# Performance work log

Hardware: AMD Instinct MI355X
Metric: run time of the kernel (lower is better)

The kernel has to match this reference:

```python
import jax, jax.numpy as jnp
import numpy as np

DIM = 768
HEADS = 12
HEAD_DIM = DIM // HEADS
SCALE = HEAD_DIM ** -0.5


def setup_inputs() -> dict:
    key = jax.random.key(0)
    ks = jax.random.split(key, 8)
    B, N = 2, 1024
    w = lambda k, shape: jax.random.normal(k, shape, dtype=jnp.float32) * (shape[0] ** -0.5)
    return {
        "x1": jax.random.normal(ks[0], (B, N, DIM), dtype=jnp.float32),
        "x2": jax.random.normal(ks[1], (B, N, DIM), dtype=jnp.float32),
        "Wqkv1": w(ks[2], (DIM, 3 * DIM)),
        "Wqkv2": w(ks[3], (DIM, 3 * DIM)),
        "Wp1": w(ks[4], (DIM, DIM)),
        "bp1": jnp.zeros((DIM,), dtype=jnp.float32),
        "Wp2": w(ks[5], (DIM, DIM)),
        "bp2": jnp.zeros((DIM,), dtype=jnp.float32),
    }


def _qkv(x, W):
    # x: [B,N,C] -> q,k,v each [B,H,N,Dh]
    B, N, C = x.shape
    out = (x @ W).reshape(B, N, 3, HEADS, HEAD_DIM)
    out = jnp.transpose(out, (2, 0, 3, 1, 4))  # [3,B,H,N,Dh]
    return out[0], out[1], out[2]


def _attn(q, k, v):
    # q: [B,H,Nq,Dh], k/v: [B,H,Nk,Dh] -> [B,Nq,H*Dh]
    scores = jnp.einsum("bhqd,bhkd->bhqk", q, k) * SCALE
    a = jax.nn.softmax(scores, axis=-1)
    o = jnp.einsum("bhqk,bhkd->bqhd", a, v)
    B, Nq = o.shape[0], o.shape[1]
    return o.reshape(B, Nq, HEADS * HEAD_DIM)


def reference(x1, x2, Wqkv1, Wqkv2, Wp1, bp1, Wp2, bp2):
    q1, k1, v1 = _qkv(x1, Wqkv1)
    q2, k2, v2 = _qkv(x2, Wqkv2)
    # four-way self+cross attention (dropout p=0 -> identity)
    o1 = _attn(q1, k1, v1) + _attn(q1, k2, v2)
    o2 = _attn(q2, k2, v2) + _attn(q2, k1, v1)
    y1 = o1 @ Wp1 + bp1
    y2 = o2 @ Wp2 + bp2
    return (y1, y2)
```

## Files before the change

### kernel.cpp

```cpp
#include <hip/hip_runtime.h>
#include <stdint.h>

#define HEADS 12
#define DH 64
#define SEQ 1024
#define BATCH 2
#define DIMC 768
#define MROWS (BATCH*SEQ)
#define NQKV (3*DIMC)

typedef __bf16 bf16x8 __attribute__((ext_vector_type(8)));
typedef float f32x4 __attribute__((ext_vector_type(4)));
typedef unsigned int u32x4 __attribute__((ext_vector_type(4)));

__device__ __forceinline__ uint16_t f2bf(float f) {
  uint32_t u = __builtin_bit_cast(uint32_t, f);
  uint32_t r = (u + 0x7fffu + ((u >> 16) & 1u)) >> 16;
  return (uint16_t)r;
}

__device__ __forceinline__ void gl16(const void* g, void* l) {
  __builtin_amdgcn_global_load_lds(
      (const __attribute__((address_space(1))) void*)g,
      (__attribute__((address_space(3))) void*)l, 16, 0, 0);
}

__global__ __launch_bounds__(256) void k_cast_x(
    const float* __restrict__ x1, const float* __restrict__ x2,
    uint16_t* __restrict__ xb) {
  int i = blockIdx.x * 256 + threadIdx.x;
  const int per = MROWS * DIMC / 4;
  const float* src = (i < per) ? x1 : x2;
  int j = (i < per) ? i : (i - per);
  float4 v = reinterpret_cast<const float4*>(src)[j];
  reinterpret_cast<ushort4*>(xb)[i] =
      make_ushort4(f2bf(v.x), f2bf(v.y), f2bf(v.z), f2bf(v.w));
}

__global__ __launch_bounds__(256) void k_transpose_all(
    const float* __restrict__ Wqkv1, const float* __restrict__ Wqkv2,
    const float* __restrict__ Wp1, const float* __restrict__ Wp2,
    uint16_t* __restrict__ wqkvt, uint16_t* __restrict__ wpt) {
  __shared__ uint16_t tile[32][33];
  int id = blockIdx.x;
  const float* src; uint16_t* dst; int C, xo, yo;
  if (id < 3456) {
    int s = id / 1728; id %= 1728;
    src = s ? Wqkv2 : Wqkv1; dst = wqkvt + (size_t)s * NQKV * DIMC; C = NQKV;
    xo = id % 72; yo = id / 72;
  } else {
    id -= 3456; int s = id / 576; id %= 576;
    src = s ? Wp2 : Wp1; dst = wpt + (size_t)s * DIMC * DIMC; C = DIMC;
    xo = id % 24; yo = id / 24;
  }
  const int R = DIMC;
  int c0 = xo * 32, r0 = yo * 32;
  int tx = threadIdx.x, ty = threadIdx.y;
  for (int rr = ty; rr < 32; rr += 8)
    tile[rr][tx] = f2bf(src[(size_t)(r0 + rr) * C + c0 + tx]);
  __syncthreads();
  for (int rr = ty; rr < 32; rr += 8)
    dst[(size_t)(c0 + rr) * R + r0 + tx] = tile[tx][rr];
}

__global__ __launch_bounds__(256) void k_qkv_gemm(
    const uint16_t* __restrict__ xb,
    const uint16_t* __restrict__ wt,
    uint16_t* __restrict__ qo, uint16_t* __restrict__ ko, uint16_t* __restrict__ vto) {
  __shared__ __align__(16) uint16_t Ax[2][128][64];
  __shared__ __align__(16) uint16_t Bt[2][64][64];

  int flat = blockIdx.x + 16 * blockIdx.y + 576 * blockIdx.z;
  flat = (flat & 7) * 144 + (flat >> 3);
  const int yb = flat % 36;
  const int xbk = (flat / 36) % 16;
  const int s  = flat / 576;
  const int m0 = xbk * 128;
  const int col0 = yb * 64;

  const uint16_t* x_s  = xb + (size_t)s * MROWS * DIMC;
  const uint16_t* wt_s = wt + (size_t)s * NQKV * DIMC;

  const int tid = threadIdx.x;
  const int w = tid >> 6, lane = tid & 63;
  const int lr = lane & 15, g = lane >> 4;
  const int srow8 = lane >> 3;
  const int schunk8 = ((lane & 7) ^ srow8) * 8;

  f32x4 acc[2][4] = {};

  size_t aoff[4], boff[2];
#pragma unroll
  for (int j = 0; j < 4; ++j)
    aoff[j] = (size_t)(m0 + w * 32 + j * 8 + srow8) * DIMC + schunk8;
#pragma unroll
  for (int j = 0; j < 2; ++j)
    boff[j] = (size_t)(col0 + w * 16 + j * 8 + srow8) * DIMC + schunk8;

#define STAGE(B, K0) do {                                  \
    gl16(x_s  + aoff[0] + (K0), &Ax[B][w * 32 +  0][0]);   \
    gl16(x_s  + aoff[1] + (K0), &Ax[B][w * 32 +  8][0]);   \
    gl16(x_s  + aoff[2] + (K0), &Ax[B][w * 32 + 16][0]);   \
    gl16(x_s  + aoff[3] + (K0), &Ax[B][w * 32 + 24][0]);   \
    gl16(wt_s + boff[0] + (K0), &Bt[B][w * 16 +  0][0]);   \
    gl16(wt_s + boff[1] + (K0), &Bt[B][w * 16 +  8][0]); } while (0)

  STAGE(0, 0);

  for (int kt = 0; kt < 12; ++kt) {
    const int cur = kt & 1;
    if (kt < 11) {
      STAGE(cur ^ 1, (kt + 1) * 64);
      asm volatile("s_waitcnt vmcnt(6)" ::: "memory");
    } else {
      asm volatile("s_waitcnt vmcnt(0)" ::: "memory");
    }
    __builtin_amdgcn_s_barrier();
    __builtin_amdgcn_sched_barrier(0);

    bf16x8 ah[2][2], bb[4][2];
#pragma unroll
    for (int fm = 0; fm < 2; ++fm)
#pragma unroll
      for (int kk = 0; kk < 2; ++kk) {
        const int ch = ((kk * 4 + g) ^ (lr & 7)) * 8;
        ah[fm][kk] = *reinterpret_cast<const bf16x8*>(&Ax[cur][w * 32 + fm * 16 + lr][ch]);
      }
#pragma unroll
    for (int fn = 0; fn < 4; ++fn)
#pragma unroll
      for (int kk = 0; kk < 2; ++kk) {
        const int ch = ((kk * 4 + g) ^ (lr & 7)) * 8;
        bb[fn][kk] = *reinterpret_cast<const bf16x8*>(&Bt[cur][fn * 16 + lr][ch]);
      }

    asm volatile("s_waitcnt lgkmcnt(0)" ::: "memory");
    __builtin_amdgcn_sched_barrier(0);
    __builtin_amdgcn_s_setprio(1);
#pragma unroll
    for (int fm = 0; fm < 2; ++fm)
#pragma unroll
      for (int fn = 0; fn < 4; ++fn)
#pragma unroll
        for (int kk = 0; kk < 2; ++kk)
          acc[fm][fn] = __builtin_amdgcn_mfma_f32_16x16x32_bf16(ah[fm][kk], bb[fn][kk], acc[fm][fn], 0, 0, 0);
    __builtin_amdgcn_s_setprio(0);
    __builtin_amdgcn_sched_barrier(0);
    __builtin_amdgcn_s_barrier();
  }
#undef STAGE

  const int t = col0 / 768;
  const int cbase = col0 % 768;
  const int h = cbase >> 6;
  uint16_t* q_s  = qo  + (size_t)s * 1572864;
  uint16_t* k_s  = ko  + (size_t)s * 1572864;
  uint16_t* vt_s = vto + (size_t)s * 1572864;
#pragma unroll
  for (int fm = 0; fm < 2; ++fm)
#pragma unroll
    for (int fn = 0; fn < 4; ++fn) {
      const int dh = fn * 16 + lr;
#pragma unroll
      for (int i = 0; i < 4; ++i) {
        int m = m0 + w * 32 + fm * 16 + g * 4 + i;
        int b_ = m >> 10, n = m & 1023;
        float v = acc[fm][fn][i];
        if (t == 0)
          q_s[((size_t)(b_ * HEADS + h) * SEQ + n) * DH + dh] = f2bf(v * 0.125f);
        else if (t == 1)
          k_s[((size_t)(b_ * HEADS + h) * SEQ + n) * DH + dh] = f2bf(v);
        else
          vt_s[((size_t)(b_ * HEADS + h) * DH + dh) * SEQ + n] = f2bf(v);
      }
    }
}

__global__ __launch_bounds__(256) void k_attn(
    const uint16_t* __restrict__ q, const uint16_t* __restrict__ k,
    const uint16_t* __restrict__ vt, uint16_t* __restrict__ o) {
  __shared__ uint16_t Klds[2][64][64];
  __shared__ uint16_t Vlds[2][64][64];

  int bid = blockIdx.x;
  bid = (bid & 7) * 96 + (bid >> 3);
  const int qt = bid & 15;
  int rest = bid >> 4;
  const int h = rest % 12;
  int rest2 = rest / 12;
  const int b = rest2 & 1;
  const int s = rest2 >> 1;

  const int tid = threadIdx.x;
  const int w = tid >> 6, lane = tid & 63;
  const int lr = lane & 15;
  const int g = lane >> 4;
  const int hi8 = g * 8;

  const uint16_t* q_s = q + (size_t)s * 1572864 +
                        ((size_t)(b * HEADS + h) * SEQ + qt * 64 + w * 16 + lr) * DH;
  const bf16x8 qf0 = *reinterpret_cast<const bf16x8*>(&q_s[hi8]);
  const bf16x8 qf1 = *reinterpret_cast<const bf16x8*>(&q_s[32 + hi8]);

  const int klo = (lr >> 2) * 8 + (lr & 3);

  const int r0 = tid >> 3;
  const int c0 = tid & 7;
  const int swc = 8 * (c0 ^ (r0 & 7));

  const uint16_t* kbase0 = k  + (size_t)s * 1572864 + (size_t)(b * HEADS + h) * SEQ * DH;
  const uint16_t* vbase0 = vt + (size_t)s * 1572864 + (size_t)(b * HEADS + h) * DH * SEQ;
  const uint16_t* kbase1 = k  + (size_t)(1 - s) * 1572864 + (size_t)(b * HEADS + h) * SEQ * DH;
  const uint16_t* vbase1 = vt + (size_t)(1 - s) * 1572864 + (size_t)(b * HEADS + h) * DH * SEQ;

  u32x4 kr0, kr1, vr0, vr1;

#define LOADT(T) { const int tt = (T); const int kt_ = tt & 15;                             \
    const uint16_t* kp = (tt >= 16) ? kbase1 : kbase0;                                      \
    const uint16_t* vp = (tt >= 16) ? vbase1 : vbase0;                                      \
    kr0 = *reinterpret_cast<const u32x4*>(&kp[(size_t)(kt_ * 64 + r0) * DH + c0 * 8]);      \
    kr1 = *reinterpret_cast<const u32x4*>(&kp[(size_t)(kt_ * 64 + r0 + 32) * DH + c0 * 8]); \
    vr0 = *reinterpret_cast<const u32x4*>(&vp[(size_t)r0 * SEQ + kt_ * 64 + c0 * 8]);       \
    vr1 = *reinterpret_cast<const u32x4*>(&vp[(size_t)(r0 + 32) * SEQ + kt_ * 64 + c0 * 8]); }

#define STORET(B) {                                              \
    *reinterpret_cast<u32x4*>(&Klds[B][r0][swc]) = kr0;          \
    *reinterpret_cast<u32x4*>(&Klds[B][r0 + 32][swc]) = kr1;     \
    *reinterpret_cast<u32x4*>(&Vlds[B][r0][swc]) = vr0;          \
    *reinterpret_cast<u32x4*>(&Vlds[B][r0 + 32][swc]) = vr1; }

  LOADT(0);
  STORET(0);
  __syncthreads();

  f32x4 Oacc[4] = {};
  f32x4 Ofin[4] = {};
  float mrow = -1e30f, lrow = 0.f;

  for (int t = 0; t < 32; ++t) {
    const int cur = t & 1;
    if (t < 31) LOADT(t + 1);

    f32x4 S[4];
    __builtin_amdgcn_s_setprio(1);
#pragma unroll
    for (int fn = 0; fn < 4; ++fn) {
      const int krow = klo + 4 * (fn & 1) + 32 * (fn >> 1);
      const int sw = krow & 7;
      bf16x8 ka = *reinterpret_cast<const bf16x8*>(&Klds[cur][krow][8 * (g ^ sw)]);
      bf16x8 kb = *reinterpret_cast<const bf16x8*>(&Klds[cur][krow][8 * ((4 + g) ^ sw)]);
      f32x4 z = {};
      z = __builtin_amdgcn_mfma_f32_16x16x32_bf16(ka, qf0, z, 0, 0, 0);
      S[fn] = __builtin_amdgcn_mfma_f32_16x16x32_bf16(kb, qf1, z, 0, 0, 0);
    }
    __builtin_amdgcn_s_setprio(0);

    float vmax = fmaxf(fmaxf(fmaxf(S[0][0], S[0][1]), fmaxf(S[0][2], S[0][3])),
                       fmaxf(fmaxf(S[1][0], S[1][1]), fmaxf(S[1][2], S[1][3])));
    vmax = fmaxf(vmax, fmaxf(fmaxf(fmaxf(S[2][0], S[2][1]), fmaxf(S[2][2], S[2][3])),
                             fmaxf(fmaxf(S[3][0], S[3][1]), fmaxf(S[3][2], S[3][3]))));
    vmax = fmaxf(vmax, __shfl_xor(vmax, 16));
    vmax = fmaxf(vmax, __shfl_xor(vmax, 32));
    const float mnew = fmaxf(mrow, vmax);
    const float alpha = __expf(mrow - mnew);
    mrow = mnew;
    float rs = 0.f;
#pragma unroll
    for (int fn = 0; fn < 4; ++fn)
#pragma unroll
      for (int i = 0; i < 4; ++i) {
        float p = __expf(S[fn][i] - mnew);
        S[fn][i] = p;
        rs += p;
      }
    rs += __shfl_xor(rs, 16);
    rs += __shfl_xor(rs, 32);
    lrow = lrow * alpha + rs;

    bf16x8 pa0, pa1;
#pragma unroll
    for (int i = 0; i < 4; ++i) {
      pa0[i]     = (__bf16)S[0][i];
      pa0[4 + i] = (__bf16)S[1][i];
      pa1[i]     = (__bf16)S[2][i];
      pa1[4 + i] = (__bf16)S[3][i];
    }

    float af[4];
#pragma unroll
    for (int i = 0; i < 4; ++i) af[i] = __shfl(alpha, 20 * g + i);
#pragma unroll
    for (int fn = 0; fn < 4; ++fn)
#pragma unroll
      for (int i = 0; i < 4; ++i) Oacc[fn][i] *= af[i];

    __builtin_amdgcn_s_setprio(1);
#pragma unroll
    for (int fn = 0; fn < 4; ++fn) {
      const int vrow = fn * 16 + lr;
      const int sw = vrow & 7;
      bf16x8 va = *reinterpret_cast<const bf16x8*>(&Vlds[cur][vrow][8 * (g ^ sw)]);
      bf16x8 vb = *reinterpret_cast<const bf16x8*>(&Vlds[cur][vrow][8 * ((4 + g) ^ sw)]);
      Oacc[fn] = __builtin_amdgcn_mfma_f32_16x16x32_bf16(pa0, va, Oacc[fn], 0, 0, 0);
      Oacc[fn] = __builtin_amdgcn_mfma_f32_16x16x32_bf16(pa1, vb, Oacc[fn], 0, 0, 0);
    }
    __builtin_amdgcn_s_setprio(0);

    if (t == 15 || t == 31) {
      const float linv = 1.f / lrow;
      float li[4];
#pragma unroll
      for (int i = 0; i < 4; ++i) li[i] = __shfl(linv, 20 * g + i);
#pragma unroll
      for (int fn = 0; fn < 4; ++fn)
#pragma unroll
        for (int i = 0; i < 4; ++i) Ofin[fn][i] += Oacc[fn][i] * li[i];
      if (t == 15) {
        mrow = -1e30f; lrow = 0.f;
#pragma unroll
        for (int fn = 0; fn < 4; ++fn) Oacc[fn] = f32x4{};
      }
    }

    if (t < 31) STORET(cur ^ 1);
    __syncthreads();
  }
#undef LOADT
#undef STORET

  uint16_t* o_s = o + (size_t)s * MROWS * DIMC;
#pragma unroll
  for (int fn = 0; fn < 4; ++fn)
#pragma unroll
    for (int i = 0; i < 4; ++i) {
      int n = qt * 64 + w * 16 + g * 4 + i;
      int col = h * 64 + fn * 16 + lr;
      o_s[(size_t)(b * SEQ + n) * DIMC + col] = f2bf(Ofin[fn][i]);
    }
}

__global__ __launch_bounds__(256) void k_proj_gemm(
    const uint16_t* __restrict__ o, const uint16_t* __restrict__ wpt,
    const float* __restrict__ bp1, const float* __restrict__ bp2,
    float* __restrict__ out) {
  __shared__ __align__(16) uint16_t At[2][128][32];
  __shared__ __align__(16) uint16_t Bt[2][64][32];

  int flat = blockIdx.x + 16 * blockIdx.y + 192 * blockIdx.z;
  flat = (flat & 7) * 48 + (flat >> 3);
  const int yb = flat % 12;
  const int xb = (flat / 12) % 16;
  const int s  = flat / 192;
  const int m0 = xb * 128;
  const int col0 = yb * 64;

  const uint16_t* o_s = o + (size_t)s * MROWS * DIMC;
  const uint16_t* w_s = wpt + (size_t)s * DIMC * DIMC;
  const float* bias = (s == 0) ? bp1 : bp2;
  float* out_s = out + (size_t)s * MROWS * DIMC;

  const int tid = threadIdx.x;
  const int w = tid >> 6, lane = tid & 63;
  const int lr = lane & 15, g = lane >> 4;
  const int pc = (g ^ ((lr >> 1) & 3)) * 8;
  const int srow = lane >> 2;
  const int schunk = ((lane & 3) ^ ((lane >> 3) & 3)) * 8;

  f32x4 acc[2][4] = {};

  const size_t aoff0 = (size_t)(m0 + w * 32 + srow) * DIMC + schunk;
  const size_t aoff1 = (size_t)(m0 + w * 32 + 16 + srow) * DIMC + schunk;
  const size_t boff  = (size_t)(col0 + w * 16 + srow) * DIMC + schunk;

#define STAGE(B, K0) do {                                      \
    gl16(o_s + aoff0 + (K0), &At[B][w * 32][0]);               \
    gl16(o_s + aoff1 + (K0), &At[B][w * 32 + 16][0]);          \
    gl16(w_s + boff  + (K0), &Bt[B][w * 16][0]); } while (0)

  STAGE(0, 0);

  for (int kt = 0; kt < 24; ++kt) {
    const int cur = kt & 1;
    if (kt < 23) {
      STAGE(cur ^ 1, (kt + 1) * 32);
      asm volatile("s_waitcnt vmcnt(3)" ::: "memory");
    } else {
      asm volatile("s_waitcnt vmcnt(0)" ::: "memory");
    }
    __builtin_amdgcn_s_barrier();
    __builtin_amdgcn_sched_barrier(0);

    bf16x8 a[2], bb[4];
#pragma unroll
    for (int f = 0; f < 2; ++f)
      a[f] = *reinterpret_cast<const bf16x8*>(&At[cur][w * 32 + f * 16 + lr][pc]);
#pragma unroll
    for (int f = 0; f < 4; ++f)
      bb[f] = *reinterpret_cast<const bf16x8*>(&Bt[cur][f * 16 + lr][pc]);

    asm volatile("s_waitcnt lgkmcnt(0)" ::: "memory");
    __builtin_amdgcn_sched_barrier(0);
    __builtin_amdgcn_s_setprio(1);
#pragma unroll
    for (int fm = 0; fm < 2; ++fm)
#pragma unroll
      for (int fn = 0; fn < 4; ++fn)
        acc[fm][fn] = __builtin_amdgcn_mfma_f32_16x16x32_bf16(a[fm], bb[fn], acc[fm][fn], 0, 0, 0);
    __builtin_amdgcn_s_setprio(0);
    __builtin_amdgcn_sched_barrier(0);
    __builtin_amdgcn_s_barrier();
  }
#undef STAGE

#pragma unroll
  for (int fm = 0; fm < 2; ++fm)
#pragma unroll
    for (int fn = 0; fn < 4; ++fn) {
      const int col = col0 + fn * 16 + lr;
      const float bv = bias[col];
#pragma unroll
      for (int i = 0; i < 4; ++i) {
        int m = m0 + w * 32 + fm * 16 + g * 4 + i;
        out_s[(size_t)m * DIMC + col] = acc[fm][fn][i] + bv;
      }
    }
}

extern "C" void kernel_launch(void* const* d_in, const int* in_sizes, int n_in,
                              void* d_out, int out_size, void* d_ws, size_t ws_size,
                              hipStream_t stream) {
  const float* x1    = (const float*)d_in[0];
  const float* x2    = (const float*)d_in[1];
  const float* Wqkv1 = (const float*)d_in[2];
  const float* Wqkv2 = (const float*)d_in[3];
  const float* Wp1   = (const float*)d_in[4];
  const float* bp1   = (const float*)d_in[5];
  const float* Wp2   = (const float*)d_in[6];
  const float* bp2   = (const float*)d_in[7];
  float* out = (float*)d_out;

  uint8_t* ws = (uint8_t*)d_ws;
  uint16_t* xbuf  = (uint16_t*)(ws);
  uint16_t* wqkvt = (uint16_t*)(ws + 12582912);
  uint16_t* wpt   = (uint16_t*)(ws + 19660800);
  uint16_t* qb    = (uint16_t*)(ws + 22020096);
  uint16_t* kb    = (uint16_t*)(ws + 28311552);
  uint16_t* vtb   = (uint16_t*)(ws + 34603008);
  uint16_t* ob    = (uint16_t*)(ws + 40894464);

  k_cast_x<<<3072, 256, 0, stream>>>(x1, x2, xbuf);
  k_transpose_all<<<4608, dim3(32, 8), 0, stream>>>(Wqkv1, Wqkv2, Wp1, Wp2, wqkvt, wpt);
  k_qkv_gemm<<<dim3(16, 36, 2), 256, 0, stream>>>(xbuf, wqkvt, qb, kb, vtb);
  k_attn<<<768, 256, 0, stream>>>(qb, kb, vtb, ob);
  k_proj_gemm<<<dim3(16, 12, 2), 256, 0, stream>>>(ob, wpt, bp1, bp2, out);
}
```

Baseline: 119.6 us.

## Use lazy softmax rescaling, new LDS swizzle, and unroll attention loop by two

The attention kernel now rescales the running max and accumulator only when a wave sees a score exceeding the current max by more than a threshold, which avoids most cross-lane shuffles and per-step rescale multiplies. The per-lane row sum is kept partial and reduced across lanes only at each pass epilogue. The K/V LDS swizzle key changes to mix higher row bits, aiming to reduce bank conflicts. The main loop is manually unrolled by two with fixed buffer indices. Lazy rescaling lets exponentials grow up to e^8 before bf16 conversion, which remains numerically safe but alters rounding.

```diff
diff --git a/kernel.cpp b/kernel.cpp
--- a/kernel.cpp
+++ b/kernel.cpp
@@ -176,6 +176,8 @@
     }
 }
 
+#define SWKEY(r) ((((r) >> 2) ^ (r)) & 7)
+
 __global__ __launch_bounds__(256) void k_attn(
     const uint16_t* __restrict__ q, const uint16_t* __restrict__ k,
     const uint16_t* __restrict__ vt, uint16_t* __restrict__ o) {
@@ -206,7 +208,7 @@
 
   const int r0 = tid >> 3;
   const int c0 = tid & 7;
-  const int swc = 8 * (c0 ^ (r0 & 7));
+  const int swck = 8 * (c0 ^ SWKEY(r0));
 
   const uint16_t* kbase0 = k  + (size_t)s * 1572864 + (size_t)(b * HEADS + h) * SEQ * DH;
   const uint16_t* vbase0 = vt + (size_t)s * 1572864 + (size_t)(b * HEADS + h) * DH * SEQ;
@@ -223,11 +225,11 @@
     vr0 = *reinterpret_cast<const u32x4*>(&vp[(size_t)r0 * SEQ + kt_ * 64 + c0 * 8]);       \
     vr1 = *reinterpret_cast<const u32x4*>(&vp[(size_t)(r0 + 32) * SEQ + kt_ * 64 + c0 * 8]); }
 
-#define STORET(B) {                                              \
-    *reinterpret_cast<u32x4*>(&Klds[B][r0][swc]) = kr0;          \
-    *reinterpret_cast<u32x4*>(&Klds[B][r0 + 32][swc]) = kr1;     \
-    *reinterpret_cast<u32x4*>(&Vlds[B][r0][swc]) = vr0;          \
-    *reinterpret_cast<u32x4*>(&Vlds[B][r0 + 32][swc]) = vr1; }
+#define STORET(B) {                                               \
+    *reinterpret_cast<u32x4*>(&Klds[B][r0][swck]) = kr0;          \
+    *reinterpret_cast<u32x4*>(&Klds[B][r0 + 32][swck]) = kr1;     \
+    *reinterpret_cast<u32x4*>(&Vlds[B][r0][swck]) = vr0;          \
+    *reinterpret_cast<u32x4*>(&Vlds[B][r0 + 32][swck]) = vr1; }
 
   LOADT(0);
   STORET(0);
@@ -237,96 +239,105 @@
   f32x4 Ofin[4] = {};
   float mrow = -1e30f, lrow = 0.f;
 
-  for (int t = 0; t < 32; ++t) {
-    const int cur = t & 1;
-    if (t < 31) LOADT(t + 1);
-
-    f32x4 S[4];
-    __builtin_amdgcn_s_setprio(1);
-#pragma unroll
-    for (int fn = 0; fn < 4; ++fn) {
-      const int krow = klo + 4 * (fn & 1) + 32 * (fn >> 1);
-      const int sw = krow & 7;
-      bf16x8 ka = *reinterpret_cast<const bf16x8*>(&Klds[cur][krow][8 * (g ^ sw)]);
-      bf16x8 kb = *reinterpret_cast<const bf16x8*>(&Klds[cur][krow][8 * ((4 + g) ^ sw)]);
-      f32x4 z = {};
-      z = __builtin_amdgcn_mfma_f32_16x16x32_bf16(ka, qf0, z, 0, 0, 0);
-      S[fn] = __builtin_amdgcn_mfma_f32_16x16x32_bf16(kb, qf1, z, 0, 0, 0);
-    }
-    __builtin_amdgcn_s_setprio(0);
-
-    float vmax = fmaxf(fmaxf(fmaxf(S[0][0], S[0][1]), fmaxf(S[0][2], S[0][3])),
-                       fmaxf(fmaxf(S[1][0], S[1][1]), fmaxf(S[1][2], S[1][3])));
-    vmax = fmaxf(vmax, fmaxf(fmaxf(fmaxf(S[2][0], S[2][1]), fmaxf(S[2][2], S[2][3])),
-                             fmaxf(fmaxf(S[3][0], S[3][1]), fmaxf(S[3][2], S[3][3]))));
-    vmax = fmaxf(vmax, __shfl_xor(vmax, 16));
-    vmax = fmaxf(vmax, __shfl_xor(vmax, 32));
-    const float mnew = fmaxf(mrow, vmax);
-    const float alpha = __expf(mrow - mnew);
-    mrow = mnew;
-    float rs = 0.f;
-#pragma unroll
-    for (int fn = 0; fn < 4; ++fn)
-#pragma unroll
-      for (int i = 0; i < 4; ++i) {
-        float p = __expf(S[fn][i] - mnew);
-        S[fn][i] = p;
-        rs += p;
-      }
-    rs += __shfl_xor(rs, 16);
-    rs += __shfl_xor(rs, 32);
-    lrow = lrow * alpha + rs;
-
-    bf16x8 pa0, pa1;
-#pragma unroll
-    for (int i = 0; i < 4; ++i) {
-      pa0[i]     = (__bf16)S[0][i];
-      pa0[4 + i] = (__bf16)S[1][i];
-      pa1[i]     = (__bf16)S[2][i];
-      pa1[4 + i] = (__bf16)S[3][i];
-    }
-
-    float af[4];
-#pragma unroll
-    for (int i = 0; i < 4; ++i) af[i] = __shfl(alpha, 20 * g + i);
-#pragma unroll
-    for (int fn = 0; fn < 4; ++fn)
-#pragma unroll
-      for (int i = 0; i < 4; ++i) Oacc[fn][i] *= af[i];
-
-    __builtin_amdgcn_s_setprio(1);
-#pragma unroll
-    for (int fn = 0; fn < 4; ++fn) {
-      const int vrow = fn * 16 + lr;
-      const int sw = vrow & 7;
-      bf16x8 va = *reinterpret_cast<const bf16x8*>(&Vlds[cur][vrow][8 * (g ^ sw)]);
-      bf16x8 vb = *reinterpret_cast<const bf16x8*>(&Vlds[cur][vrow][8 * ((4 + g) ^ sw)]);
-      Oacc[fn] = __builtin_amdgcn_mfma_f32_16x16x32_bf16(pa0, va, Oacc[fn], 0, 0, 0);
-      Oacc[fn] = __builtin_amdgcn_mfma_f32_16x16x32_bf16(pa1, vb, Oacc[fn], 0, 0, 0);
-    }
-    __builtin_amdgcn_s_setprio(0);
-
-    if (t == 15 || t == 31) {
-      const float linv = 1.f / lrow;
-      float li[4];
-#pragma unroll
-      for (int i = 0; i < 4; ++i) li[i] = __shfl(linv, 20 * g + i);
-#pragma unroll
-      for (int fn = 0; fn < 4; ++fn)
-#pragma unroll
-        for (int i = 0; i < 4; ++i) Ofin[fn][i] += Oacc[fn][i] * li[i];
-      if (t == 15) {
-        mrow = -1e30f; lrow = 0.f;
-#pragma unroll
-        for (int fn = 0; fn < 4; ++fn) Oacc[fn] = f32x4{};
-      }
-    }
-
-    if (t < 31) STORET(cur ^ 1);
+#define COMPUTE(CUR)                                                              \
+  {                                                                               \
+    f32x4 S[4];                                                                   \
+    __builtin_amdgcn_s_setprio(1);                                                \
+    _Pragma("unroll")                                                             \
+    for (int fn = 0; fn < 4; ++fn) {                                              \
+      const int krow = klo + 4 * (fn & 1) + 32 * (fn >> 1);                       \
+      const int sw = SWKEY(krow);                                                 \
+      bf16x8 ka = *reinterpret_cast<const bf16x8*>(&Klds[CUR][krow][8 * (g ^ sw)]);        \
+      bf16x8 kb = *reinterpret_cast<const bf16x8*>(&Klds[CUR][krow][8 * ((4 + g) ^ sw)]);  \
+      f32x4 z = {};                                                               \
+      z = __builtin_amdgcn_mfma_f32_16x16x32_bf16(ka, qf0, z, 0, 0, 0);           \
+      S[fn] = __builtin_amdgcn_mfma_f32_16x16x32_bf16(kb, qf1, z, 0, 0, 0);       \
+    }                                                                             \
+    __builtin_amdgcn_s_setprio(0);                                                \
+    float t0_ = fmaxf(fmaxf(S[0][0], S[0][1]), S[0][2]);                          \
+    float t1_ = fmaxf(fmaxf(S[0][3], S[1][0]), S[1][1]);                          \
+    float t2_ = fmaxf(fmaxf(S[1][2], S[1][3]), S[2][0]);                          \
+    float t3_ = fmaxf(fmaxf(S[2][1], S[2][2]), S[2][3]);                          \
+    float t4_ = fmaxf(fmaxf(S[3][0], S[3][1]), S[3][2]);                          \
+    float own_ = fmaxf(fmaxf(fmaxf(t0_, t1_), t2_),                               \
+                       fmaxf(fmaxf(t3_, t4_), S[3][3]));                          \
+    if (__any(own_ > mrow + 8.0f)) {           \
+      float pmax = fmaxf(own_, __shfl_xor(own_, 16));                             \
+      pmax = fmaxf(pmax, __shfl_xor(pmax, 32));                                   \
+      const float mnew = fmaxf(mrow, pmax);                                       \
+      const float alpha = __expf(mrow - mnew);                                    \
+      float af0 = __shfl(alpha, 20 * g + 0), af1 = __shfl(alpha, 20 * g + 1);     \
+      float af2 = __shfl(alpha, 20 * g + 2), af3 = __shfl(alpha, 20 * g + 3);     \
+      _Pragma("unroll")                                                           \
+      for (int fn = 0; fn < 4; ++fn) {                                            \
+        Oacc[fn][0] *= af0; Oacc[fn][1] *= af1;                                   \
+        Oacc[fn][2] *= af2; Oacc[fn][3] *= af3;                                   \
+      }                                                                           \
+      lrow *= alpha; mrow = mnew;                                                 \
+    }                                                                             \
+    float rs0 = 0.f, rs1 = 0.f, rs2 = 0.f, rs3 = 0.f;                             \
+    _Pragma("unroll")                                                             \
+    for (int i = 0; i < 4; ++i) {                                                 \
+      float p0 = __expf(S[0][i] - mrow), p1 = __expf(S[1][i] - mrow);             \
+      float p2 = __expf(S[2][i] - mrow), p3 = __expf(S[3][i] - mrow);             \
+      S[0][i] = p0; S[1][i] = p1; S[2][i] = p2; S[3][i] = p3;                     \
+      rs0 += p0; rs1 += p1; rs2 += p2; rs3 += p3;                                 \
+    }                                                                             \
+    lrow += (rs0 + rs1) + (rs2 + rs3);                                            \
+    bf16x8 pa0, pa1;                                                              \
+    _Pragma("unroll")                                                             \
+    for (int i = 0; i < 4; ++i) {                                                 \
+      pa0[i] = (__bf16)S[0][i]; pa0[4 + i] = (__bf16)S[1][i];                     \
+      pa1[i] = (__bf16)S[2][i]; pa1[4 + i] = (__bf16)S[3][i];                     \
+    }                                                                             \
+    __builtin_amdgcn_s_setprio(1);                                                \
+    _Pragma("unroll")                                                             \
+    for (int fn = 0; fn < 4; ++fn) {                                              \
+      const int vrow = fn * 16 + lr;                                              \
+      const int sw = SWKEY(vrow);                                                 \
+      bf16x8 va = *reinterpret_cast<const bf16x8*>(&Vlds[CUR][vrow][8 * (g ^ sw)]);        \
+      bf16x8 vb = *reinterpret_cast<const bf16x8*>(&Vlds[CUR][vrow][8 * ((4 + g) ^ sw)]);  \
+      Oacc[fn] = __builtin_amdgcn_mfma_f32_16x16x32_bf16(pa0, va, Oacc[fn], 0, 0, 0);      \
+      Oacc[fn] = __builtin_amdgcn_mfma_f32_16x16x32_bf16(pa1, vb, Oacc[fn], 0, 0, 0);      \
+    }                                                                             \
+    __builtin_amdgcn_s_setprio(0);                                                \
+  }
+
+#define PASS_EPI(RESET)                                                           \
+  {                                                                               \
+    float lsum = lrow + __shfl_xor(lrow, 16);                                     \
+    lsum += __shfl_xor(lsum, 32);                                                 \
+    const float linv = 1.f / lsum;                                                \
+    float li0 = __shfl(linv, 20 * g + 0), li1 = __shfl(linv, 20 * g + 1);         \
+    float li2 = __shfl(linv, 20 * g + 2), li3 = __shfl(linv, 20 * g + 3);         \
+    _Pragma("unroll")                                                             \
+    for (int fn = 0; fn < 4; ++fn) {                                              \
+      Ofin[fn][0] += Oacc[fn][0] * li0; Ofin[fn][1] += Oacc[fn][1] * li1;         \
+      Ofin[fn][2] += Oacc[fn][2] * li2; Ofin[fn][3] += Oacc[fn][3] * li3;         \
+    }                                                                             \
+    if (RESET) {                                                                  \
+      mrow = -1e30f; lrow = 0.f;                                                  \
+      _Pragma("unroll") for (int fn = 0; fn < 4; ++fn) Oacc[fn] = f32x4{};        \
+    }                                                                             \
+  }
+
+#pragma unroll 1
+  for (int t2 = 0; t2 < 16; ++t2) {
+    LOADT(2 * t2 + 1);
+    COMPUTE(0);
+    STORET(1);
+    __syncthreads();
+    if (t2 < 15) LOADT(2 * t2 + 2);
+    COMPUTE(1);
+    if (t2 == 7)  PASS_EPI(1);
+    if (t2 == 15) PASS_EPI(0);
+    if (t2 < 15) STORET(0);
     __syncthreads();
   }
 #undef LOADT
 #undef STORET
+#undef COMPUTE
+#undef PASS_EPI
 
   uint16_t* o_s = o + (size_t)s * MROWS * DIMC;
 #pragma unroll
```

Result: faster. 109.9 us (-8.1%).
